# Kernel tuning notes

Measured on AMD Instinct MI355X. Metric: run time of the kernel, lower is better.

Reference implementation:

```python
import jax, jax.numpy as jnp
import numpy as np

D = 256      # embed_dims
NH = 8       # num_heads
NL = 1       # num_levels
NP = 6       # num_points
BS = 1
NQ = 40000   # 200x200 BEV queries
H0, W0 = 200, 200
HD = D // NH


def _ln(x, g, b):
    m = jnp.mean(x, -1, keepdims=True)
    v = jnp.var(x, -1, keepdims=True)
    return (x - m) / jnp.sqrt(v + 1e-5) * g + b


def _bilinear(v, lx, ly, H, W):
    # v: (bs, h, H*W, hd); lx/ly: (bs, h, S) pixel coords (align_corners=False, zero padding)
    x0 = jnp.floor(lx).astype(jnp.int32)
    y0 = jnp.floor(ly).astype(jnp.int32)
    acc = 0.
    for dx in (0, 1):
        for dy in (0, 1):
            xi = x0 + dx
            yi = y0 + dy
            w = (1. - jnp.abs(lx - xi)) * (1. - jnp.abs(ly - yi))
            valid = (xi >= 0) & (xi < W) & (yi >= 0) & (yi < H)
            idx = jnp.clip(yi, 0, H - 1) * W + jnp.clip(xi, 0, W - 1)
            g = jnp.take_along_axis(v, idx[..., None], axis=2)  # (bs,h,S,hd)
            acc = acc + g * (w * valid)[..., None]
    return acc


def _forward(query, value, reference_points, W_off, b_off, W_attn, b_attn,
             W_val, b_val, W_out, b_out, ln1_g, ln1_b, W1, b1, W2, b2,
             ln2_g, ln2_b, ss, lsi):
    bs, nq, d = query.shape
    # sampling offsets and attention weights from the query
    off = (query @ W_off + b_off).reshape(bs, nq, NH, NL, NP, 2)
    attn = jax.nn.softmax((query @ W_attn + b_attn).reshape(bs, nq, NH, NL * NP), -1)
    attn = attn.reshape(bs, nq, NH, NL, NP)
    v = (value @ W_val + b_val).reshape(bs, -1, NH, HD).transpose(0, 2, 1, 3)  # (bs,h,HW,hd)
    # offset normalizer is [W, H] per level
    norm = jnp.stack([ss[:, 1], ss[:, 0]], -1).astype(query.dtype)  # (NL,2)
    loc = reference_points[:, :, None, :, None, :] + off / norm[None, None, None, :, None, :]
    out = jnp.zeros((bs, NH, nq, HD), query.dtype)
    for l in range(NL):
        Hl = int(ss[l, 0]); Wl = int(ss[l, 1]); st = int(lsi[l])
        vl = v[:, :, st:st + Hl * Wl]
        lx = (loc[:, :, :, l, :, 0] * Wl - 0.5).transpose(0, 2, 1, 3).reshape(bs, NH, nq * NP)
        ly = (loc[:, :, :, l, :, 1] * Hl - 0.5).transpose(0, 2, 1, 3).reshape(bs, NH, nq * NP)
        sampled = _bilinear(vl, lx, ly, Hl, Wl).reshape(bs, NH, nq, NP, HD)
        wl = attn[:, :, :, l, :].transpose(0, 2, 1, 3)  # (bs,h,nq,P)
        out = out + jnp.einsum('bhqp,bhqpd->bhqd', wl, sampled)
    y_msda = out.transpose(0, 2, 1, 3).reshape(bs, nq, d) @ W_out + b_out
    y = _ln(y_msda + query, ln1_g, ln1_b)
    y_ffn = jax.nn.gelu(y @ W1 + b1, approximate=False) @ W2 + b2
    return _ln(y_ffn + y, ln2_g, ln2_b)


def setup_inputs():
    key = jax.random.key(0)
    ks = jax.random.split(key, 12)
    s = 0.02
    return {
        'query': jax.random.normal(ks[0], (BS, NQ, D), jnp.float32),
        'value': jax.random.normal(ks[1], (BS, H0 * W0, D), jnp.float32),
        'reference_points': jax.random.uniform(ks[2], (BS, NQ, NL, 2), jnp.float32),
        'spatial_shapes': jnp.array([[H0, W0]], jnp.int32),
        'level_start_index': jnp.array([0], jnp.int32),
        'W_off': jax.random.normal(ks[3], (D, NH * NL * NP * 2), jnp.float32) * s,
        'b_off': jax.random.uniform(ks[4], (NH * NL * NP * 2,), jnp.float32, -1., 1.),
        'W_attn': jax.random.normal(ks[5], (D, NH * NL * NP), jnp.float32) * s,
        'b_attn': jnp.zeros((NH * NL * NP,), jnp.float32),
        'W_val': jax.random.normal(ks[6], (D, D), jnp.float32) * s,
        'b_val': jnp.zeros((D,), jnp.float32),
        'W_out': jax.random.normal(ks[7], (D, D), jnp.float32) * s,
        'b_out': jnp.zeros((D,), jnp.float32),
        'ln1_g': jnp.ones((D,), jnp.float32),
        'ln1_b': jnp.zeros((D,), jnp.float32),
        'W1': jax.random.normal(ks[8], (D, D), jnp.float32) * s,
        'b1': jnp.zeros((D,), jnp.float32),
        'W2': jax.random.normal(ks[9], (D, D), jnp.float32) * s,
        'b2': jnp.zeros((D,), jnp.float32),
        'ln2_g': jnp.ones((D,), jnp.float32),
        'ln2_b': jnp.zeros((D,), jnp.float32),
    }


def reference(query, value, reference_points, spatial_shapes, level_start_index,
              W_off, b_off, W_attn, b_attn, W_val, b_val, W_out, b_out,
              ln1_g, ln1_b, W1, b1, W2, b2, ln2_g, ln2_b):
    ss = np.asarray(spatial_shapes)
    lsi = np.asarray(level_start_index)
    return _forward(query, value, reference_points, W_off, b_off, W_attn, b_attn,
                    W_val, b_val, W_out, b_out, ln1_g, ln1_b, W1, b1, W2, b2,
                    ln2_g, ln2_b, ss, lsi)
```

## Files before the change

### kernel.cpp

```cpp
#include <hip/hip_runtime.h>
#include <math.h>

#define NQ 40000
#define DIM 256
#define NH 8
#define NP 6
#define HD 32
#define GH 200
#define GW 200

typedef short bf16x8 __attribute__((ext_vector_type(8)));
typedef float f32x4 __attribute__((ext_vector_type(4)));

__device__ __forceinline__ unsigned short f2bf(float f) {
    unsigned int u = __builtin_bit_cast(unsigned int, f);
    u += 0x7fffu + ((u >> 16) & 1u);
    return (unsigned short)(u >> 16);
}
__device__ __forceinline__ float bf2f(unsigned short h) {
    return __builtin_bit_cast(float, ((unsigned int)h) << 16);
}

__global__ void __launch_bounds__(256)
f2b_kernel(const float* __restrict__ src, unsigned short* __restrict__ dst, int n8) {
    const int i = blockIdx.x * 256 + threadIdx.x;
    if (i >= n8) return;
    const float4* s = (const float4*)src;
    float4 a = s[(size_t)i * 2], b = s[(size_t)i * 2 + 1];
    bf16x8 o;
    o[0] = (short)f2bf(a.x); o[1] = (short)f2bf(a.y);
    o[2] = (short)f2bf(a.z); o[3] = (short)f2bf(a.w);
    o[4] = (short)f2bf(b.x); o[5] = (short)f2bf(b.y);
    o[6] = (short)f2bf(b.z); o[7] = (short)f2bf(b.w);
    *(bf16x8*)(dst + (size_t)i * 8) = o;
}

__global__ void __launch_bounds__(256)
wtrans_kernel(const float* __restrict__ Wval, const float* __restrict__ Woff,
              const float* __restrict__ Wattn, const float* __restrict__ Wout,
              const float* __restrict__ W1, const float* __restrict__ W2,
              const float* __restrict__ b_off, const float* __restrict__ b_attn,
              unsigned short* __restrict__ Bt, float* __restrict__ bias_oa) {
    __shared__ float T[64][65];
    const int m = blockIdx.z;
    const float* src; int N; int dr0;
    if (m == 0)      { src = Wval;  N = 256; dr0 = 0; }
    else if (m == 1) { src = Woff;  N = 96;  dr0 = 256; }
    else if (m == 2) { src = Wattn; N = 48;  dr0 = 352; }
    else if (m == 3) { src = Wout;  N = 256; dr0 = 400; }
    else if (m == 4) { src = W1;    N = 256; dr0 = 656; }
    else             { src = W2;    N = 256; dr0 = 912; }

    if (m == 1 && blockIdx.x == 0 && blockIdx.y == 0 && threadIdx.x < 144)
        bias_oa[threadIdx.x] = threadIdx.x < 96 ? b_off[threadIdx.x]
                                                : b_attn[threadIdx.x - 96];

    const int n0 = blockIdx.x * 64, k0 = blockIdx.y * 64;
    if (n0 >= N) return;
    const int col = threadIdx.x & 63, rg = threadIdx.x >> 6;
#pragma unroll
    for (int i = 0; i < 16; ++i) {
        const int r = rg + 4 * i;
        T[r][col] = (n0 + col < N) ? src[(size_t)(k0 + r) * N + n0 + col] : 0.0f;
    }
    __syncthreads();
#pragma unroll
    for (int i = 0; i < 16; ++i) {
        const int nl = rg + 4 * i;
        if (n0 + nl < N)
            Bt[(size_t)(dr0 + n0 + nl) * 256 + k0 + col] = f2bf(T[col][nl]);
    }
}

template <int EPI>
__global__ void __launch_bounds__(256)
gemm_bt(const unsigned short* __restrict__ A, const unsigned short* __restrict__ Bt,
        const float* __restrict__ bias, void* __restrict__ C,
        int M, int N, int ldc) {
    __shared__ __align__(16) unsigned short As[128 * 32];
    __shared__ __align__(16) unsigned short Bs[128 * 32];

    const int tid = threadIdx.x, lane = tid & 63, wave = tid >> 6;
    const int quad = lane >> 4, l16 = lane & 15;
    const int wm = wave >> 1, wn = wave & 1;
    const int bm0 = blockIdx.y * 128, bn0 = blockIdx.x * 128;

    f32x4 acc[4][4] = {};

    const int rl = lane >> 2;
    const int c8 = (lane & 3) * 8;

    for (int kt = 0; kt < 8; ++kt) {
        const int k0 = kt * 32;
        __syncthreads();
#pragma unroll
        for (int i = 0; i < 2; ++i) {
            const int rgrp = i * 64 + wave * 16;
            const int gA = min(bm0 + rgrp + rl, M - 1);
            const unsigned short* gpa = A + (size_t)gA * 256 + k0 + c8;
            __builtin_amdgcn_global_load_lds(
                (const __attribute__((address_space(1))) void*)gpa,
                (__attribute__((address_space(3))) void*)(As + (size_t)rgrp * 32),
                16, 0, 0);
            const int gB = min(bn0 + rgrp + rl, N - 1);
            const unsigned short* gpb = Bt + (size_t)gB * 256 + k0 + c8;
            __builtin_amdgcn_global_load_lds(
                (const __attribute__((address_space(1))) void*)gpb,
                (__attribute__((address_space(3))) void*)(Bs + (size_t)rgrp * 32),
                16, 0, 0);
        }
        __syncthreads();

        bf16x8 af[4], bw[4];
#pragma unroll
        for (int t = 0; t < 4; ++t) {
            af[t] = *(const bf16x8*)&As[(wm * 64 + t * 16 + l16) * 32 + quad * 8];
            bw[t] = *(const bf16x8*)&Bs[(wn * 64 + t * 16 + l16) * 32 + quad * 8];
        }
#pragma unroll
        for (int tm = 0; tm < 4; ++tm)
#pragma unroll
            for (int tn = 0; tn < 4; ++tn)
                acc[tm][tn] = __builtin_amdgcn_mfma_f32_16x16x32_bf16(
                    af[tm], bw[tn], acc[tm][tn], 0, 0, 0);
    }

#pragma unroll
    for (int tm = 0; tm < 4; ++tm) {
        const int row0 = bm0 + wm * 64 + tm * 16 + quad * 4;
#pragma unroll
        for (int tn = 0; tn < 4; ++tn) {
            const int col = bn0 + wn * 64 + tn * 16 + l16;
            if (col < N) {
                const float bv = bias[col];
#pragma unroll
                for (int r = 0; r < 4; ++r) {
                    const int row = row0 + r;
                    if (row < M) {
                        float x = acc[tm][tn][r] + bv;
                        if (EPI == 1) {
                            x = 0.5f * x * (1.0f + erff(x * 0.70710678118654752f));
                            ((unsigned short*)C)[(size_t)row * ldc + col] = f2bf(x);
                        } else if (EPI == 2) {
                            ((unsigned short*)C)[(size_t)row * ldc + col] = f2bf(x);
                        } else {
                            ((float*)C)[(size_t)row * ldc + col] = x;
                        }
                    }
                }
            }
        }
    }
}

__global__ void __launch_bounds__(256)
msda_sample(const unsigned short* __restrict__ v,
            const unsigned short* __restrict__ oa,
            const float* __restrict__ rp,
            unsigned short* __restrict__ out) {
    const int tid = threadIdx.x;
    const int slot = tid >> 2;
    const int q = blockIdx.x * 8 + (slot >> 3);
    const int h = slot & 7;
    const int c0 = (tid & 3) * 8;

    const float rx = rp[q * 2 + 0] * (float)GW;
    const float ry = rp[q * 2 + 1] * (float)GH;

    const unsigned short* oaq = oa + (size_t)q * 144;
    float lg[NP];
    float mx = -1e30f;
#pragma unroll
    for (int p = 0; p < NP; ++p) {
        lg[p] = bf2f(oaq[96 + h * NP + p]);
        mx = fmaxf(mx, lg[p]);
    }
    float s = 0.0f;
#pragma unroll
    for (int p = 0; p < NP; ++p) { lg[p] = expf(lg[p] - mx); s += lg[p]; }
    const float inv = 1.0f / s;

    float acc[8] = {};
#pragma unroll
    for (int p = 0; p < NP; ++p) {
        const float aw = lg[p] * inv;
        const float lx = rx + bf2f(oaq[h * 12 + p * 2 + 0]) - 0.5f;
        const float ly = ry + bf2f(oaq[h * 12 + p * 2 + 1]) - 0.5f;
        const float fx0 = floorf(lx), fy0 = floorf(ly);
        const int x0 = (int)fx0, y0 = (int)fy0;
        const float fx = lx - fx0, fy = ly - fy0;
#pragma unroll
        for (int dy = 0; dy < 2; ++dy) {
            const int yi = y0 + dy;
            const float wyv = dy ? fy : 1.0f - fy;
#pragma unroll
            for (int dx = 0; dx < 2; ++dx) {
                const int xi = x0 + dx;
                const float wxv = dx ? fx : 1.0f - fx;
                const bool valid = (xi >= 0) & (xi < GW) & (yi >= 0) & (yi < GH);
                const int yc = min(max(yi, 0), GH - 1);
                const int xc = min(max(xi, 0), GW - 1);
                const float w = valid ? aw * wxv * wyv : 0.0f;
                const bf16x8 g = *(const bf16x8*)&v[((size_t)(yc * GW + xc)) * 256 + h * 32 + c0];
#pragma unroll
                for (int j = 0; j < 8; ++j)
                    acc[j] += bf2f((unsigned short)g[j]) * w;
            }
        }
    }
    bf16x8 o;
#pragma unroll
    for (int j = 0; j < 8; ++j) o[j] = (short)f2bf(acc[j]);
    *(bf16x8*)&out[(size_t)q * 256 + h * 32 + c0] = o;
}

__global__ void __launch_bounds__(256)
ln_res(const float* __restrict__ x, const float* __restrict__ res,
       const float* __restrict__ g, const float* __restrict__ b,
       float* __restrict__ out, unsigned short* __restrict__ out_bf, int M) {
    const int wave = threadIdx.x >> 6;
    const int lane = threadIdx.x & 63;
    const int row = blockIdx.x * 4 + wave;
    if (row >= M) return;

    const size_t base = (size_t)row * DIM + lane * 4;
    const float4 xv = *(const float4*)(x + base);
    const float4 rv = *(const float4*)(res + base);
    float e[4] = {xv.x + rv.x, xv.y + rv.y, xv.z + rv.z, xv.w + rv.w};

    float s = e[0] + e[1] + e[2] + e[3];
    float sq = e[0] * e[0] + e[1] * e[1] + e[2] * e[2] + e[3] * e[3];
#pragma unroll
    for (int o = 1; o < 64; o <<= 1) {
        s += __shfl_xor(s, o);
        sq += __shfl_xor(sq, o);
    }
    const float mean = s * (1.0f / DIM);
    const float var = sq * (1.0f / DIM) - mean * mean;
    const float rstd = rsqrtf(var + 1e-5f);

    const float4 gv = *(const float4*)(g + lane * 4);
    const float4 bv = *(const float4*)(b + lane * 4);
    float4 o4;
    o4.x = (e[0] - mean) * rstd * gv.x + bv.x;
    o4.y = (e[1] - mean) * rstd * gv.y + bv.y;
    o4.z = (e[2] - mean) * rstd * gv.z + bv.z;
    o4.w = (e[3] - mean) * rstd * gv.w + bv.w;
    *(float4*)(out + base) = o4;
    if (out_bf) {
        bf16x8 ob;
        ob[0] = (short)f2bf(o4.x); ob[1] = (short)f2bf(o4.y);
        ob[2] = (short)f2bf(o4.z); ob[3] = (short)f2bf(o4.w);
        *(uint2*)(out_bf + base) = *(uint2*)&ob;
    }
}

extern "C" void kernel_launch(void* const* d_in, const int* in_sizes, int n_in,
                              void* d_out, int out_size, void* d_ws, size_t ws_size,
                              hipStream_t stream) {
    const float* query  = (const float*)d_in[0];
    const float* value  = (const float*)d_in[1];
    const float* rp     = (const float*)d_in[2];
    const float* W_off  = (const float*)d_in[5];
    const float* b_off  = (const float*)d_in[6];
    const float* W_attn = (const float*)d_in[7];
    const float* b_attn = (const float*)d_in[8];
    const float* W_val  = (const float*)d_in[9];
    const float* b_val  = (const float*)d_in[10];
    const float* W_out  = (const float*)d_in[11];
    const float* b_out  = (const float*)d_in[12];
    const float* ln1_g  = (const float*)d_in[13];
    const float* ln1_b  = (const float*)d_in[14];
    const float* W1     = (const float*)d_in[15];
    const float* b1     = (const float*)d_in[16];
    const float* W2     = (const float*)d_in[17];
    const float* b2     = (const float*)d_in[18];
    const float* ln2_g  = (const float*)d_in[19];
    const float* ln2_b  = (const float*)d_in[20];

    char* ws = (char*)d_ws;
    unsigned short* Bt       = (unsigned short*)ws;
    float*          bias_oa  = (float*)(ws + 598016);
    unsigned short* query_bf = (unsigned short*)(ws + 655360);
    unsigned short* h1_bf    = query_bf;
    unsigned short* value_bf = (unsigned short*)(ws + 21135360);
    unsigned short* msda_bf  = value_bf;
    unsigned short* y_bf     = value_bf;
    unsigned short* v_bf     = (unsigned short*)(ws + 41615360);
    unsigned short* oa_bf    = (unsigned short*)(ws + 62095360);
    float*          y        = (float*)(ws + 41615360);
    float*          outp     = (float*)d_out;

    dim3 blk(256);
    f2b_kernel<<<dim3(5000), blk, 0, stream>>>(query, query_bf, 1280000);
    f2b_kernel<<<dim3(5000), blk, 0, stream>>>(value, value_bf, 1280000);
    wtrans_kernel<<<dim3(4, 4, 6), blk, 0, stream>>>(W_val, W_off, W_attn, W_out, W1, W2,
                                                     b_off, b_attn, Bt, bias_oa);
    gemm_bt<2><<<dim3(2, 313), blk, 0, stream>>>(value_bf, Bt, b_val, (void*)v_bf, NQ, 256, 256);
    gemm_bt<2><<<dim3(2, 313), blk, 0, stream>>>(query_bf, Bt + 256 * 256, bias_oa,
                                                 (void*)oa_bf, NQ, 144, 144);
    msda_sample<<<dim3(5000), blk, 0, stream>>>(v_bf, oa_bf, rp, msda_bf);
    gemm_bt<0><<<dim3(2, 313), blk, 0, stream>>>(msda_bf, Bt + 400 * 256, b_out,
                                                 (void*)outp, NQ, 256, 256);
    ln_res<<<dim3(10000), blk, 0, stream>>>(outp, query, ln1_g, ln1_b, y, y_bf, NQ);
    gemm_bt<1><<<dim3(2, 313), blk, 0, stream>>>(y_bf, Bt + 656 * 256, b1,
                                                 (void*)h1_bf, NQ, 256, 256);
    gemm_bt<0><<<dim3(2, 313), blk, 0, stream>>>(h1_bf, Bt + 912 * 256, b2,
                                                 (void*)outp, NQ, 256, 256);
    ln_res<<<dim3(10000), blk, 0, stream>>>(outp, y, ln2_g, ln2_b, outp, nullptr, NQ);
}
```

Measured before the change: 368.4 us.

## Sort queries by spatial tile for MSDA locality, merge casts, keep LN residual bf16

```diff
diff --git a/kernel.cpp b/kernel.cpp
--- a/kernel.cpp
+++ b/kernel.cpp
@@ -8,6 +8,9 @@
 #define HD 32
 #define GH 200
 #define GW 200
+#define TS 8
+#define TNX 25
+#define NT 625
 
 typedef short bf16x8 __attribute__((ext_vector_type(8)));
 typedef float f32x4 __attribute__((ext_vector_type(4)));
@@ -22,16 +25,19 @@
 }
 
 __global__ void __launch_bounds__(256)
-f2b_kernel(const float* __restrict__ src, unsigned short* __restrict__ dst, int n8) {
-    const int i = blockIdx.x * 256 + threadIdx.x;
-    if (i >= n8) return;
+f2b_kernel(const float* __restrict__ q, unsigned short* __restrict__ qd,
+           const float* __restrict__ v, unsigned short* __restrict__ vd) {
+    int b = blockIdx.x;
+    const float* src; unsigned short* dst;
+    if (b < 5000) { src = q; dst = qd; } else { src = v; dst = vd; b -= 5000; }
+    const int i = b * 256 + threadIdx.x;
     const float4* s = (const float4*)src;
-    float4 a = s[(size_t)i * 2], b = s[(size_t)i * 2 + 1];
+    float4 a = s[(size_t)i * 2], c = s[(size_t)i * 2 + 1];
     bf16x8 o;
     o[0] = (short)f2bf(a.x); o[1] = (short)f2bf(a.y);
     o[2] = (short)f2bf(a.z); o[3] = (short)f2bf(a.w);
-    o[4] = (short)f2bf(b.x); o[5] = (short)f2bf(b.y);
-    o[6] = (short)f2bf(b.z); o[7] = (short)f2bf(b.w);
+    o[4] = (short)f2bf(c.x); o[5] = (short)f2bf(c.y);
+    o[6] = (short)f2bf(c.z); o[7] = (short)f2bf(c.w);
     *(bf16x8*)(dst + (size_t)i * 8) = o;
 }
 
@@ -70,6 +76,60 @@
         if (n0 + nl < N)
             Bt[(size_t)(dr0 + n0 + nl) * 256 + k0 + col] = f2bf(T[col][nl]);
     }
+}
+
+__device__ __forceinline__ int tile_of(const float* rp, int q) {
+    const float rx = rp[q * 2 + 0] * (float)GW;
+    const float ry = rp[q * 2 + 1] * (float)GH;
+    const int tx = min(max((int)(rx * (1.0f / TS)), 0), TNX - 1);
+    const int ty = min(max((int)(ry * (1.0f / TS)), 0), TNX - 1);
+    return ty * TNX + tx;
+}
+
+__global__ void __launch_bounds__(256)
+sort_zero(int* __restrict__ hist) {
+    const int i = blockIdx.x * 256 + threadIdx.x;
+    if (i < NT) hist[i] = 0;
+}
+
+__global__ void __launch_bounds__(256)
+sort_hist(const float* __restrict__ rp, int* __restrict__ hist) {
+    const int q = blockIdx.x * 256 + threadIdx.x;
+    if (q >= NQ) return;
+    atomicAdd(&hist[tile_of(rp, q)], 1);
+}
+
+__global__ void __launch_bounds__(64)
+sort_scan(const int* __restrict__ hist, int* __restrict__ cursor) {
+    const int lane = threadIdx.x;
+    int loc[10]; int t = 0;
+#pragma unroll
+    for (int j = 0; j < 10; ++j) {
+        const int idx = lane * 10 + j;
+        loc[j] = t;
+        t += (idx < NT) ? hist[idx] : 0;
+    }
+    int s = t;
+#pragma unroll
+    for (int o = 1; o < 64; o <<= 1) {
+        const int u = __shfl_up(s, o);
+        if (lane >= o) s += u;
+    }
+    const int ex = s - t;
+#pragma unroll
+    for (int j = 0; j < 10; ++j) {
+        const int idx = lane * 10 + j;
+        if (idx < NT) cursor[idx] = ex + loc[j];
+    }
+}
+
+__global__ void __launch_bounds__(256)
+sort_scatter(const float* __restrict__ rp, int* __restrict__ cursor,
+             int* __restrict__ perm) {
+    const int q = blockIdx.x * 256 + threadIdx.x;
+    if (q >= NQ) return;
+    const int pos = atomicAdd(&cursor[tile_of(rp, q)], 1);
+    perm[pos] = q;
 }
 
 template <int EPI>
@@ -157,10 +217,13 @@
 msda_sample(const unsigned short* __restrict__ v,
             const unsigned short* __restrict__ oa,
             const float* __restrict__ rp,
+            const int* __restrict__ perm,
             unsigned short* __restrict__ out) {
+    const int b = blockIdx.x;
+    const int w = (b & 7) * 625 + (b >> 3);
     const int tid = threadIdx.x;
     const int slot = tid >> 2;
-    const int q = blockIdx.x * 8 + (slot >> 3);
+    const int q = perm[w * 8 + (slot >> 3)];
     const int h = slot & 7;
     const int c0 = (tid & 3) * 8;
 
@@ -200,11 +263,11 @@
                 const bool valid = (xi >= 0) & (xi < GW) & (yi >= 0) & (yi < GH);
                 const int yc = min(max(yi, 0), GH - 1);
                 const int xc = min(max(xi, 0), GW - 1);
-                const float w = valid ? aw * wxv * wyv : 0.0f;
+                const float wgt = valid ? aw * wxv * wyv : 0.0f;
                 const bf16x8 g = *(const bf16x8*)&v[((size_t)(yc * GW + xc)) * 256 + h * 32 + c0];
 #pragma unroll
                 for (int j = 0; j < 8; ++j)
-                    acc[j] += bf2f((unsigned short)g[j]) * w;
+                    acc[j] += bf2f((unsigned short)g[j]) * wgt;
             }
         }
     }
@@ -214,10 +277,11 @@
     *(bf16x8*)&out[(size_t)q * 256 + h * 32 + c0] = o;
 }
 
-__global__ void __launch_bounds__(256)
-ln_res(const float* __restrict__ x, const float* __restrict__ res,
+template <int RES_BF, int OUT_BF>
+__global__ void __launch_bounds__(256)
+ln_res(const float* __restrict__ x, const void* __restrict__ res,
        const float* __restrict__ g, const float* __restrict__ b,
-       float* __restrict__ out, unsigned short* __restrict__ out_bf, int M) {
+       void* __restrict__ out, int M) {
     const int wave = threadIdx.x >> 6;
     const int lane = threadIdx.x & 63;
     const int row = blockIdx.x * 4 + wave;
@@ -225,8 +289,18 @@
 
     const size_t base = (size_t)row * DIM + lane * 4;
     const float4 xv = *(const float4*)(x + base);
-    const float4 rv = *(const float4*)(res + base);
-    float e[4] = {xv.x + rv.x, xv.y + rv.y, xv.z + rv.z, xv.w + rv.w};
+    float e[4];
+    if (RES_BF) {
+        const unsigned short* rb = (const unsigned short*)res + base;
+        uint2 rv = *(const uint2*)rb;
+        const unsigned short* rs = (const unsigned short*)&rv;
+        e[0] = xv.x + bf2f(rs[0]); e[1] = xv.y + bf2f(rs[1]);
+        e[2] = xv.z + bf2f(rs[2]); e[3] = xv.w + bf2f(rs[3]);
+    } else {
+        const float4 rv = *(const float4*)((const float*)res + base);
+        e[0] = xv.x + rv.x; e[1] = xv.y + rv.y;
+        e[2] = xv.z + rv.z; e[3] = xv.w + rv.w;
+    }
 
     float s = e[0] + e[1] + e[2] + e[3];
     float sq = e[0] * e[0] + e[1] * e[1] + e[2] * e[2] + e[3] * e[3];
@@ -241,17 +315,16 @@
 
     const float4 gv = *(const float4*)(g + lane * 4);
     const float4 bv = *(const float4*)(b + lane * 4);
-    float4 o4;
-    o4.x = (e[0] - mean) * rstd * gv.x + bv.x;
-    o4.y = (e[1] - mean) * rstd * gv.y + bv.y;
-    o4.z = (e[2] - mean) * rstd * gv.z + bv.z;
-    o4.w = (e[3] - mean) * rstd * gv.w + bv.w;
-    *(float4*)(out + base) = o4;
-    if (out_bf) {
-        bf16x8 ob;
-        ob[0] = (short)f2bf(o4.x); ob[1] = (short)f2bf(o4.y);
-        ob[2] = (short)f2bf(o4.z); ob[3] = (short)f2bf(o4.w);
-        *(uint2*)(out_bf + base) = *(uint2*)&ob;
+    float o0 = (e[0] - mean) * rstd * gv.x + bv.x;
+    float o1 = (e[1] - mean) * rstd * gv.y + bv.y;
+    float o2 = (e[2] - mean) * rstd * gv.z + bv.z;
+    float o3 = (e[3] - mean) * rstd * gv.w + bv.w;
+    if (OUT_BF) {
+        unsigned short ob[4] = {f2bf(o0), f2bf(o1), f2bf(o2), f2bf(o3)};
+        *(uint2*)((unsigned short*)out + base) = *(uint2*)ob;
+    } else {
+        float4 o4 = {o0, o1, o2, o3};
+        *(float4*)((float*)out + base) = o4;
     }
 }
 
@@ -281,31 +354,36 @@
     char* ws = (char*)d_ws;
     unsigned short* Bt       = (unsigned short*)ws;
     float*          bias_oa  = (float*)(ws + 598016);
-    unsigned short* query_bf = (unsigned short*)(ws + 655360);
+    int*            hist     = (int*)(ws + 598592);
+    int*            cursor   = (int*)(ws + 601600);
+    int*            perm     = (int*)(ws + 604608);
+    unsigned short* query_bf = (unsigned short*)(ws + 770048);
     unsigned short* h1_bf    = query_bf;
-    unsigned short* value_bf = (unsigned short*)(ws + 21135360);
+    unsigned short* value_bf = (unsigned short*)(ws + 21250048);
     unsigned short* msda_bf  = value_bf;
     unsigned short* y_bf     = value_bf;
-    unsigned short* v_bf     = (unsigned short*)(ws + 41615360);
-    unsigned short* oa_bf    = (unsigned short*)(ws + 62095360);
-    float*          y        = (float*)(ws + 41615360);
+    unsigned short* v_bf     = (unsigned short*)(ws + 41730048);
+    unsigned short* oa_bf    = (unsigned short*)(ws + 62210048);
     float*          outp     = (float*)d_out;
 
     dim3 blk(256);
-    f2b_kernel<<<dim3(5000), blk, 0, stream>>>(query, query_bf, 1280000);
-    f2b_kernel<<<dim3(5000), blk, 0, stream>>>(value, value_bf, 1280000);
+    f2b_kernel<<<dim3(10000), blk, 0, stream>>>(query, query_bf, value, value_bf);
     wtrans_kernel<<<dim3(4, 4, 6), blk, 0, stream>>>(W_val, W_off, W_attn, W_out, W1, W2,
                                                      b_off, b_attn, Bt, bias_oa);
+    sort_zero<<<dim3(3), blk, 0, stream>>>(hist);
+    sort_hist<<<dim3(157), blk, 0, stream>>>(rp, hist);
+    sort_scan<<<dim3(1), dim3(64), 0, stream>>>(hist, cursor);
+    sort_scatter<<<dim3(157), blk, 0, stream>>>(rp, cursor, perm);
     gemm_bt<2><<<dim3(2, 313), blk, 0, stream>>>(value_bf, Bt, b_val, (void*)v_bf, NQ, 256, 256);
     gemm_bt<2><<<dim3(2, 313), blk, 0, stream>>>(query_bf, Bt + 256 * 256, bias_oa,
                                                  (void*)oa_bf, NQ, 144, 144);
-    msda_sample<<<dim3(5000), blk, 0, stream>>>(v_bf, oa_bf, rp, msda_bf);
+    msda_sample<<<dim3(5000), blk, 0, stream>>>(v_bf, oa_bf, rp, perm, msda_bf);
     gemm_bt<0><<<dim3(2, 313), blk, 0, stream>>>(msda_bf, Bt + 400 * 256, b_out,
                                                  (void*)outp, NQ, 256, 256);
-    ln_res<<<dim3(10000), blk, 0, stream>>>(outp, query, ln1_g, ln1_b, y, y_bf, NQ);
+    ln_res<0, 1><<<dim3(10000), blk, 0, stream>>>(outp, query, ln1_g, ln1_b, (void*)y_bf, NQ);
     gemm_bt<1><<<dim3(2, 313), blk, 0, stream>>>(y_bf, Bt + 656 * 256, b1,
                                                  (void*)h1_bf, NQ, 256, 256);
     gemm_bt<0><<<dim3(2, 313), blk, 0, stream>>>(h1_bf, Bt + 912 * 256, b2,
                                                  (void*)outp, NQ, 256, 256);
-    ln_res<<<dim3(10000), blk, 0, stream>>>(outp, y, ln2_g, ln2_b, outp, nullptr, NQ);
-}
+    ln_res<1, 0><<<dim3(10000), blk, 0, stream>>>(outp, y_bf, ln2_g, ln2_b, (void*)outp, NQ);
+}
```

New measurement: 357.4 us. 1.03x faster.
